# Kernel tuning notes

Hardware: AMD Instinct MI355X
Metric: run time of the kernel (lower is better)

Reference implementation:

```python
import jax, jax.numpy as jnp
import numpy as np

B, C, N, K = 2, 128, 4096, 16
DIM, PH, AH = 256, 64, 1024  # dim, pos_hidden_dim, dim*attn_hidden_multiplier
EPS = 1e-5

def _p(k, shape, scale=0.02):
    return jax.random.normal(k, shape, dtype=jnp.float32) * scale

def setup_inputs() -> dict:
    key0 = jax.random.key(0)
    ks = jax.random.split(key0, 32)
    d = {
        'pos': jax.random.normal(ks[0], (B, 3, N), dtype=jnp.float32),
        'key': jax.random.normal(ks[1], (B, C, N), dtype=jnp.float32),
        'query': jax.random.normal(ks[2], (B, C, N), dtype=jnp.float32),
        # MLP_Res on concat(key,query): in=2C, hidden=C, out=C
        'mlpv_w1': _p(ks[3], (C, 2 * C)), 'mlpv_b1': jnp.zeros((C,)),
        'mlpv_w2': _p(ks[4], (C, C)),     'mlpv_b2': jnp.zeros((C,)),
        'mlpv_ws': _p(ks[5], (C, 2 * C)), 'mlpv_bs': jnp.zeros((C,)),
        'wk': _p(ks[6], (DIM, C)), 'bk': jnp.zeros((DIM,)),
        'wq': _p(ks[7], (DIM, C)), 'bq': jnp.zeros((DIM,)),
        'wv': _p(ks[8], (DIM, C)), 'bv': jnp.zeros((DIM,)),
        # pos_mlp: Conv2d(3,PH,1) -> BN -> ReLU -> Conv2d(PH,DIM,1)
        'pos_w1': _p(ks[9], (PH, 3)),   'pos_b1': jnp.zeros((PH,)),
        'pos_g1': jnp.ones((PH,)),      'pos_be1': jnp.zeros((PH,)),
        'pos_w2': _p(ks[10], (DIM, PH)),'pos_b2': jnp.zeros((DIM,)),
        # attn_mlp: Conv2d(DIM,AH,1) -> BN -> ReLU -> Conv2d(AH,DIM,1)
        'att_w1': _p(ks[11], (AH, DIM)), 'att_b1': jnp.zeros((AH,)),
        'att_g1': jnp.ones((AH,)),       'att_be1': jnp.zeros((AH,)),
        'att_w2': _p(ks[12], (DIM, AH)), 'att_b2': jnp.zeros((DIM,)),
        'we': _p(ks[13], (C, DIM)), 'be': jnp.zeros((C,)),
    }
    return d

def conv1d(w, b, x):  # 1x1 conv: (o,i),(B,i,N)->(B,o,N)
    return jnp.einsum('oi,bin->bon', w, x) + b[None, :, None]

def conv2d(w, b, x):  # 1x1 conv: (o,i),(B,i,N,K)->(B,o,N,K)
    return jnp.einsum('oi,bink->bonk', w, x) + b[None, :, None, None]

def bn2d(g, be, x):  # training-mode batchnorm over (B,N,K) per channel
    m = x.mean(axis=(0, 2, 3), keepdims=True)
    v = x.var(axis=(0, 2, 3), keepdims=True)
    return g[None, :, None, None] * (x - m) * jax.lax.rsqrt(v + EPS) + be[None, :, None, None]

def knn_idx(pos, k):  # pos: (B,3,N) -> idx (B,N,k) of k nearest (incl. self)
    sq = jnp.sum(pos * pos, axis=1)                      # (B,N)
    d2 = sq[:, :, None] + sq[:, None, :] - 2.0 * jnp.einsum('bdn,bdm->bnm', pos, pos)
    _, idx = jax.lax.top_k(-d2, k)                       # smallest distances
    return idx

def group(x, idx):  # x:(B,C,N), idx:(B,N,K) -> (B,C,N,K)
    return jax.vmap(lambda xb, ib: xb[:, ib])(x, idx)

def reference(pos, key, query,
              mlpv_w1, mlpv_b1, mlpv_w2, mlpv_b2, mlpv_ws, mlpv_bs,
              wk, bk, wq, bq, wv, bv,
              pos_w1, pos_b1, pos_g1, pos_be1, pos_w2, pos_b2,
              att_w1, att_b1, att_g1, att_be1, att_w2, att_b2,
              we, be):
    x = jnp.concatenate([key, query], axis=1)            # (B,2C,N)
    value = conv1d(mlpv_w2, mlpv_b2, jax.nn.relu(conv1d(mlpv_w1, mlpv_b1, x))) \
            + conv1d(mlpv_ws, mlpv_bs, x)                # MLP_Res -> (B,C,N)
    identity = value
    k_f = conv1d(wk, bk, key)                            # (B,DIM,N)
    q_f = conv1d(wq, bq, query)
    v_f = conv1d(wv, bv, value)
    idx = knn_idx(pos, K)                                # (B,N,K)
    key_g = group(k_f, idx)                              # (B,DIM,N,K)
    qk_rel = q_f[:, :, :, None] - key_g
    pos_rel = pos[:, :, :, None] - group(pos, idx)       # (B,3,N,K)
    pos_emb = conv2d(pos_w2, pos_b2,
                     jax.nn.relu(bn2d(pos_g1, pos_be1, conv2d(pos_w1, pos_b1, pos_rel))))
    attn = conv2d(att_w2, att_b2,
                  jax.nn.relu(bn2d(att_g1, att_be1, conv2d(att_w1, att_b1, qk_rel + pos_emb))))
    attn = jax.nn.softmax(attn, axis=-1)                 # softmax over K neighbors
    v = v_f[:, :, :, None] + pos_emb                     # (B,DIM,N,K)
    agg = jnp.einsum('bcik,bcik->bci', attn, v)          # (B,DIM,N)
    y = conv1d(we, be, agg)
    return y + identity
```

## Files before the change

kernel.cpp:

```cpp
#include <hip/hip_runtime.h>
#include <math.h>

#define BB 2
#define CC 128
#define NN 4096
#define KK 16
#define DIMD 256
#define PHH 64
#define AHH 1024
#define EPSF 1e-5f
#define RSPLIT 128
#define RKCH ((BB * NN * KK) / RSPLIT)
#define LSTR 258
#define KNN_CAP 512
#define FPT 8

typedef unsigned short ushort_t;
typedef unsigned char uchar_t;
typedef unsigned long long u64;
typedef long long i64;
typedef __attribute__((ext_vector_type(8))) short short8;
typedef __attribute__((ext_vector_type(8))) unsigned short u16x8;
typedef __attribute__((ext_vector_type(4))) unsigned short u16x4;
typedef __attribute__((ext_vector_type(2))) unsigned short u16x2;
typedef __attribute__((ext_vector_type(4))) float f32x4;

__device__ __forceinline__ ushort_t f2b(float x) {
    union { float f; unsigned u; } v; v.f = x;
    unsigned r = v.u + 0x7fff + ((v.u >> 16) & 1);
    return (ushort_t)(r >> 16);
}
__device__ __forceinline__ float b2f(ushort_t x) {
    union { unsigned u; float f; } v; v.u = ((unsigned)x) << 16;
    return v.f;
}
__device__ __forceinline__ unsigned fsort(float x) {
    union { float f; unsigned u; } v; v.f = x;
    return v.u ^ ((v.u >> 31) ? 0xFFFFFFFFu : 0x80000000u);
}
__device__ __forceinline__ uchar_t f2f8(float x) {
    int p = __builtin_amdgcn_cvt_pk_fp8_f32(x, x, 0, false);
    return (uchar_t)(p & 0xFF);
}

#define GLDS16(gp, lp) __builtin_amdgcn_global_load_lds( \
    (const __attribute__((address_space(1))) void*)(gp), \
    (__attribute__((address_space(3))) void*)(lp), 16, 0, 0)

__global__ void zero_kernel(float* p, int n) {
    int i = blockIdx.x * blockDim.x + threadIdx.x;
    if (i < n) p[i] = 0.f;
}

__global__ __launch_bounds__(256) void knn_kernel(const float* __restrict__ pos,
                                                  int* __restrict__ idx) {
    int bid = blockIdx.x;
    int b = bid / NN, n = bid % NN;
    int t = threadIdx.x;
    int lane = t & 63, w = t >> 6;
    const float* px = pos + (size_t)b * 3 * NN;
    const float* py = px + NN;
    const float* pz = px + 2 * NN;
    float qx = px[n], qy = py[n], qz = pz[n];
    float qs = qx * qx + qy * qy + qz * qz;

    u64 keys[KK];
    u64 lmin = ~0ull;
#pragma unroll
    for (int j = 0; j < KK; ++j) {
        int m = t + 256 * j;
        float mx = px[m], my = py[m], mz = pz[m];
        float ms = mx * mx + my * my + mz * mz;
        float dt = qx * mx + qy * my + qz * mz;
        float d = qs + ms - 2.f * dt;
        u64 k = ((u64)fsort(d) << 32) | (unsigned)m;
        keys[j] = k;
        lmin = k < lmin ? k : lmin;
    }

    __shared__ u64 T0s[4];
    __shared__ u64 pool[KNN_CAP];
    __shared__ int cnt;

    u64 k = lmin, m4 = 0;
#pragma unroll
    for (int r = 0; r < 4; ++r) {
        u64 mv = k;
#pragma unroll
        for (int off = 32; off >= 1; off >>= 1) {
            u64 o = __shfl_xor(mv, off);
            mv = o < mv ? o : mv;
        }
        if (r == 3) m4 = mv;
        if (k == mv) k = ~0ull;
    }
    if (lane == 0) T0s[w] = m4;
    if (t == 0) cnt = 0;
    __syncthreads();
    u64 T0 = T0s[0];
    T0 = T0s[1] > T0 ? T0s[1] : T0;
    T0 = T0s[2] > T0 ? T0s[2] : T0;
    T0 = T0s[3] > T0 ? T0s[3] : T0;

#pragma unroll
    for (int j = 0; j < KK; ++j) {
        if (keys[j] <= T0) {
            int p = atomicAdd(&cnt, 1);
            if (p < KNN_CAP) pool[p] = keys[j];
        }
    }
    __syncthreads();
    int C = cnt < KNN_CAP ? cnt : KNN_CAP;
    if (t < C) {
        u64 me = pool[t];
        int r = 0;
        for (int i = 0; i < C; ++i) r += (pool[i] < me);
        if (r < KK) idx[(size_t)bid * KK + r] = (int)(me & 0xFFFFFFFFu);
    }
}

__global__ __launch_bounds__(256) void cvtx_kernel(const float* __restrict__ key,
                                                   const float* __restrict__ query,
                                                   ushort_t* __restrict__ kqT) {
    __shared__ float xs[128][65];
    int b = blockIdx.y, n0 = blockIdx.x * 64, t = threadIdx.x;
    for (int h = 0; h < 2; ++h) {
        const float* src = (h ? query : key) + (size_t)b * CC * NN;
        if (h) __syncthreads();
#pragma unroll
        for (int it = 0; it < 32; ++it) {
            int l = it * 256 + t;
            xs[l >> 6][l & 63] = src[(size_t)(l >> 6) * NN + n0 + (l & 63)];
        }
        __syncthreads();
#pragma unroll
        for (int it = 0; it < 8; ++it) {
            int l = it * 256 + t;
            int row = l >> 5, c0 = (l & 31) * 4;
            u16x4 pk;
            pk[0] = f2b(xs[c0][row]);
            pk[1] = f2b(xs[c0 + 1][row]);
            pk[2] = f2b(xs[c0 + 2][row]);
            pk[3] = f2b(xs[c0 + 3][row]);
            *(u16x4*)(kqT + ((size_t)b * NN + n0 + row) * 256 + h * 128 + c0) = pk;
        }
    }
}

template <int KLOOP, int ASTR, int EPI, int OSTR>
__global__ __launch_bounds__(256) void gemmT_kernel(const ushort_t* __restrict__ A,
                                                    const ushort_t* __restrict__ Bm,
                                                    const float* __restrict__ bias,
                                                    float* __restrict__ outF,
                                                    ushort_t* __restrict__ outB) {
    __shared__ ushort_t lA[128 * 32];
    __shared__ ushort_t lB[128 * 32];
    int t = threadIdx.x, lane = t & 63, w = t >> 6;
    int wr = w >> 1, wc = w & 1;
    size_t row0 = (size_t)blockIdx.x * 128;
    int col0 = blockIdx.y * 128;
    int m16 = lane & 15, kg = lane >> 4;
    f32x4 acc[4][4];
#pragma unroll
    for (int i = 0; i < 4; ++i)
#pragma unroll
        for (int j = 0; j < 4; ++j) acc[i][j] = (f32x4){0.f, 0.f, 0.f, 0.f};

    const ushort_t* gA = A + (row0 + (size_t)w * 16 + m16) * ASTR + kg * 8;
    const ushort_t* gB = Bm + ((size_t)(col0 + w * 16 + m16)) * KLOOP + kg * 8;
    ushort_t* lA0 = lA + w * 512;
    ushort_t* lB0 = lB + w * 512;
    for (int kt = 0; kt < KLOOP / 32; ++kt) {
        int ko = kt * 32;
        GLDS16(gA + ko, lA0);
        GLDS16(gA + (size_t)64 * ASTR + ko, lA0 + 2048);
        GLDS16(gB + ko, lB0);
        GLDS16(gB + (size_t)64 * KLOOP + ko, lB0 + 2048);
        __syncthreads();
        short8 af[4], bf[4];
#pragma unroll
        for (int i = 0; i < 4; ++i) {
            af[i] = *(const short8*)(lA + ((wr * 4 + i) * 512 + kg * 128 + m16 * 8));
            bf[i] = *(const short8*)(lB + ((wc * 4 + i) * 512 + kg * 128 + m16 * 8));
        }
#pragma unroll
        for (int i = 0; i < 4; ++i)
#pragma unroll
            for (int j = 0; j < 4; ++j)
                acc[i][j] = __builtin_amdgcn_mfma_f32_16x16x32_bf16(af[i], bf[j], acc[i][j], 0, 0, 0);
        __syncthreads();
    }
#pragma unroll
    for (int j = 0; j < 4; ++j) {
        int n = col0 + wc * 64 + j * 16 + m16;
        float bi = bias[n];
#pragma unroll
        for (int i = 0; i < 4; ++i) {
            size_t r = row0 + wr * 64 + i * 16 + kg * 4;
#pragma unroll
            for (int rg = 0; rg < 4; ++rg) {
                float v = acc[i][j][rg] + bi;
                if (EPI == 0) outB[(r + rg) * (size_t)OSTR + n] = f2b(fmaxf(v, 0.f));
                else          outF[(r + rg) * (size_t)OSTR + n] = v;
            }
        }
    }
}

__global__ __launch_bounds__(256) void gemmval_kernel(const ushort_t* __restrict__ kqT,
                                                      const ushort_t* __restrict__ h1T,
                                                      const ushort_t* __restrict__ wsb,
                                                      const ushort_t* __restrict__ w2vb,
                                                      const float* __restrict__ b2,
                                                      const float* __restrict__ bs,
                                                      float* __restrict__ valueTf,
                                                      ushort_t* __restrict__ valueTb) {
    __shared__ ushort_t lA[128 * 32];
    __shared__ ushort_t lB[128 * 32];
    int t = threadIdx.x, lane = t & 63, w = t >> 6;
    int wr = w >> 1, wc = w & 1;
    size_t row0 = (size_t)blockIdx.x * 128;
    int m16 = lane & 15, kg = lane >> 4;
    f32x4 acc[4][4];
#pragma unroll
    for (int i = 0; i < 4; ++i)
#pragma unroll
        for (int j = 0; j < 4; ++j) acc[i][j] = (f32x4){0.f, 0.f, 0.f, 0.f};
    ushort_t* lA0 = lA + w * 512;
    ushort_t* lB0 = lB + w * 512;

    {
        const ushort_t* gA = kqT + (row0 + (size_t)w * 16 + m16) * 256 + kg * 8;
        const ushort_t* gB = wsb + ((size_t)(w * 16 + m16)) * 256 + kg * 8;
        for (int kt = 0; kt < 8; ++kt) {
            int ko = kt * 32;
            GLDS16(gA + ko, lA0);
            GLDS16(gA + (size_t)64 * 256 + ko, lA0 + 2048);
            GLDS16(gB + ko, lB0);
            GLDS16(gB + (size_t)64 * 256 + ko, lB0 + 2048);
            __syncthreads();
            short8 af[4], bf[4];
#pragma unroll
            for (int i = 0; i < 4; ++i) {
                af[i] = *(const short8*)(lA + ((wr * 4 + i) * 512 + kg * 128 + m16 * 8));
                bf[i] = *(const short8*)(lB + ((wc * 4 + i) * 512 + kg * 128 + m16 * 8));
            }
#pragma unroll
            for (int i = 0; i < 4; ++i)
#pragma unroll
                for (int j = 0; j < 4; ++j)
                    acc[i][j] = __builtin_amdgcn_mfma_f32_16x16x32_bf16(af[i], bf[j], acc[i][j], 0, 0, 0);
            __syncthreads();
        }
    }
    {
        const ushort_t* gA = h1T + (row0 + (size_t)w * 16 + m16) * 128 + kg * 8;
        const ushort_t* gB = w2vb + ((size_t)(w * 16 + m16)) * 128 + kg * 8;
        for (int kt = 0; kt < 4; ++kt) {
            int ko = kt * 32;
            GLDS16(gA + ko, lA0);
            GLDS16(gA + (size_t)64 * 128 + ko, lA0 + 2048);
            GLDS16(gB + ko, lB0);
            GLDS16(gB + (size_t)64 * 128 + ko, lB0 + 2048);
            __syncthreads();
            short8 af[4], bf[4];
#pragma unroll
            for (int i = 0; i < 4; ++i) {
                af[i] = *(const short8*)(lA + ((wr * 4 + i) * 512 + kg * 128 + m16 * 8));
                bf[i] = *(const short8*)(lB + ((wc * 4 + i) * 512 + kg * 128 + m16 * 8));
            }
#pragma unroll
            for (int i = 0; i < 4; ++i)
#pragma unroll
                for (int j = 0; j < 4; ++j)
                    acc[i][j] = __builtin_amdgcn_mfma_f32_16x16x32_bf16(af[i], bf[j], acc[i][j], 0, 0, 0);
            __syncthreads();
        }
    }
#pragma unroll
    for (int j = 0; j < 4; ++j) {
        int n = wc * 64 + j * 16 + m16;
        float bi = b2[n] + bs[n];
#pragma unroll
        for (int i = 0; i < 4; ++i) {
            size_t r = row0 + wr * 64 + i * 16 + kg * 4;
#pragma unroll
            for (int rg = 0; rg < 4; ++rg) {
                float v = acc[i][j][rg] + bi;
                valueTf[(r + rg) * (size_t)CC + n] = v;
                valueTb[(r + rg) * (size_t)CC + n] = f2b(v);
            }
        }
    }
}

__global__ __launch_bounds__(256) void gemmkq_kernel(const ushort_t* __restrict__ kqT,
                                                     const ushort_t* __restrict__ wkb,
                                                     const ushort_t* __restrict__ wqb,
                                                     const float* __restrict__ bk,
                                                     const float* __restrict__ bq,
                                                     float* __restrict__ kT,
                                                     float* __restrict__ qT) {
    __shared__ ushort_t lA[128 * 32];
    __shared__ ushort_t lB[128 * 32];
    int half = blockIdx.y >> 1;
    int col0 = (blockIdx.y & 1) * 128;
    const ushort_t* A = kqT + half * 128;
    const ushort_t* Bm = half ? wqb : wkb;
    const float* bias = half ? bq : bk;
    float* outF = half ? qT : kT;

    int t = threadIdx.x, lane = t & 63, w = t >> 6;
    int wr = w >> 1, wc = w & 1;
    size_t row0 = (size_t)blockIdx.x * 128;
    int m16 = lane & 15, kg = lane >> 4;
    f32x4 acc[4][4];
#pragma unroll
    for (int i = 0; i < 4; ++i)
#pragma unroll
        for (int j = 0; j < 4; ++j) acc[i][j] = (f32x4){0.f, 0.f, 0.f, 0.f};
    const ushort_t* gA = A + (row0 + (size_t)w * 16 + m16) * 256 + kg * 8;
    const ushort_t* gB = Bm + ((size_t)(col0 + w * 16 + m16)) * 128 + kg * 8;
    ushort_t* lA0 = lA + w * 512;
    ushort_t* lB0 = lB + w * 512;
    for (int kt = 0; kt < 4; ++kt) {
        int ko = kt * 32;
        GLDS16(gA + ko, lA0);
        GLDS16(gA + (size_t)64 * 256 + ko, lA0 + 2048);
        GLDS16(gB + ko, lB0);
        GLDS16(gB + (size_t)64 * 128 + ko, lB0 + 2048);
        __syncthreads();
        short8 af[4], bf[4];
#pragma unroll
        for (int i = 0; i < 4; ++i) {
            af[i] = *(const short8*)(lA + ((wr * 4 + i) * 512 + kg * 128 + m16 * 8));
            bf[i] = *(const short8*)(lB + ((wc * 4 + i) * 512 + kg * 128 + m16 * 8));
        }
#pragma unroll
        for (int i = 0; i < 4; ++i)
#pragma unroll
            for (int j = 0; j < 4; ++j)
                acc[i][j] = __builtin_amdgcn_mfma_f32_16x16x32_bf16(af[i], bf[j], acc[i][j], 0, 0, 0);
        __syncthreads();
    }
#pragma unroll
    for (int j = 0; j < 4; ++j) {
        int n = col0 + wc * 64 + j * 16 + m16;
        float bi = bias[n];
#pragma unroll
        for (int i = 0; i < 4; ++i) {
            size_t r = row0 + wr * 64 + i * 16 + kg * 4;
#pragma unroll
            for (int rg = 0; rg < 4; ++rg)
                outF[(r + rg) * (size_t)DIMD + n] = acc[i][j][rg] + bi;
        }
    }
}

__global__ __launch_bounds__(256) void pos_stats_kernel(const float* __restrict__ pos,
                                                        const int* __restrict__ idx,
                                                        float* __restrict__ stats) {
    int sid = blockIdx.x * 256 + threadIdx.x;
    int b = sid / (NN * KK);
    int r = sid % (NN * KK);
    int n = r / KK;
    int m = idx[sid];
    const float* px = pos + (size_t)b * 3 * NN;
    float dx = px[n] - px[m];
    float dy = px[NN + n] - px[NN + m];
    float dz = px[2 * NN + n] - px[2 * NN + m];
    float v[9] = {dx, dy, dz, dx * dx, dy * dy, dz * dz, dx * dy, dx * dz, dy * dz};
    __shared__ float red[256];
    for (int j = 0; j < 9; ++j) {
        red[threadIdx.x] = v[j];
        __syncthreads();
        for (int off = 128; off >= 1; off >>= 1) {
            if (threadIdx.x < off) red[threadIdx.x] += red[threadIdx.x + off];
            __syncthreads();
        }
        if (threadIdx.x == 0) atomicAdd(&stats[j], red[0]);
        __syncthreads();
    }
}

__global__ void pos_bn_kernel(const float* __restrict__ stats, const float* __restrict__ pw1,
                              const float* __restrict__ pb1, const float* __restrict__ pg1,
                              const float* __restrict__ pbe1, float* __restrict__ posA) {
    int c = threadIdx.x;
    if (c >= PHH) return;
    float M = (float)(BB * NN * KK);
    float mu0 = stats[0] / M, mu1 = stats[1] / M, mu2 = stats[2] / M;
    float E00 = stats[3] / M, E11 = stats[4] / M, E22 = stats[5] / M;
    float E01 = stats[6] / M, E02 = stats[7] / M, E12 = stats[8] / M;
    float w0 = pw1[c * 3], w1 = pw1[c * 3 + 1], w2 = pw1[c * 3 + 2];
    float wmu = w0 * mu0 + w1 * mu1 + w2 * mu2;
    float mean_h = wmu + pb1[c];
    float Eh2 = w0 * w0 * E00 + w1 * w1 * E11 + w2 * w2 * E22
              + 2.f * (w0 * w1 * E01 + w0 * w2 * E02 + w1 * w2 * E12)
              + 2.f * pb1[c] * wmu + pb1[c] * pb1[c];
    float var = Eh2 - mean_h * mean_h;
    float a1 = pg1[c] * rsqrtf(var + EPSF);
    posA[c] = a1;
    posA[PHH + c] = pbe1[c] - mean_h * a1;
}

__global__ __launch_bounds__(256) void p1_kernel(const float* __restrict__ pos,
                                                 const int* __restrict__ idx,
                                                 const float* __restrict__ pw1,
                                                 const float* __restrict__ pb1,
                                                 const float* __restrict__ posA,
                                                 ushort_t* __restrict__ p1) {
    int gid = blockIdx.x * 256 + threadIdx.x;
    int samp = gid >> 6, c = gid & 63;
    int p = samp >> 4;
    int b = p >> 12, n = p & (NN - 1);
    int m = idx[samp];
    const float* px = pos + (size_t)b * 3 * NN;
    float dx = px[n] - px[m];
    float dy = px[NN + n] - px[NN + m];
    float dz = px[2 * NN + n] - px[2 * NN + m];
    float h = pw1[c * 3] * dx + pw1[c * 3 + 1] * dy + pw1[c * 3 + 2] * dz + pb1[c];
    p1[gid] = f2b(fmaxf(h * posA[c] + posA[PHH + c], 0.f));
}

__global__ __launch_bounds__(256) void mu_kernel(const ushort_t* __restrict__ sb16,
                                                 float* __restrict__ mu) {
    __shared__ float red[8][DIMD];
    int t = threadIdx.x;
    int rg = t >> 5;
    int c0 = (t & 31) * 8;
    const ushort_t* p = sb16 + ((size_t)blockIdx.x * 512 + rg * 64) * DIMD + c0;
    float a0 = 0.f, a1 = 0.f, a2 = 0.f, a3 = 0.f, a4 = 0.f, a5 = 0.f, a6 = 0.f, a7 = 0.f;
    for (int i = 0; i < 64; ++i) {
        u16x8 v = *(const u16x8*)(p + (size_t)i * DIMD);
        a0 += b2f(v[0]); a1 += b2f(v[1]); a2 += b2f(v[2]); a3 += b2f(v[3]);
        a4 += b2f(v[4]); a5 += b2f(v[5]); a6 += b2f(v[6]); a7 += b2f(v[7]);
    }
    red[rg][c0] = a0; red[rg][c0 + 1] = a1; red[rg][c0 + 2] = a2; red[rg][c0 + 3] = a3;
    red[rg][c0 + 4] = a4; red[rg][c0 + 5] = a5; red[rg][c0 + 6] = a6; red[rg][c0 + 7] = a7;
    __syncthreads();
    float s = 0.f;
#pragma unroll
    for (int g = 0; g < 8; ++g) s += red[g][t];
    atomicAdd(&mu[t], s);
}

__global__ __launch_bounds__(256) void rg_kernel(const ushort_t* __restrict__ S,
                                                 float* __restrict__ Rpart) {
    __shared__ ushort_t ls[32 * LSTR];
    int t = threadIdx.x;
    int lane = t & 63, w = t >> 6;
    int wr = w >> 1, wc = w & 1;
    int ti = blockIdx.y >> 1, tj = blockIdx.y & 1;
    int m16 = lane & 15, kg = lane >> 4;
    size_t kbase = (size_t)blockIdx.x * RKCH;

    f32x4 acc[4][4];
#pragma unroll
    for (int i = 0; i < 4; ++i)
#pragma unroll
        for (int j = 0; j < 4; ++j) acc[i][j] = (f32x4){0.f, 0.f, 0.f, 0.f};

    int lm = t >> 3;
    int lc = (t & 7) * 32;
    const ushort_t* gS = S + (kbase + lm) * DIMD + lc;
    ushort_t* lp = ls + lm * LSTR + lc;

    for (int kt = 0; kt < RKCH / 32; ++kt) {
        const ushort_t* gp = gS + (size_t)kt * 32 * DIMD;
        u16x8 v0 = *(const u16x8*)(gp);
        u16x8 v1 = *(const u16x8*)(gp + 8);
        u16x8 v2 = *(const u16x8*)(gp + 16);
        u16x8 v3 = *(const u16x8*)(gp + 24);
        __syncthreads();
#pragma unroll
        for (int q = 0; q < 4; ++q) {
            *(u16x2*)(lp + 0 + 2 * q) = (u16x2){v0[2 * q], v0[2 * q + 1]};
            *(u16x2*)(lp + 8 + 2 * q) = (u16x2){v1[2 * q], v1[2 * q + 1]};
            *(u16x2*)(lp + 16 + 2 * q) = (u16x2){v2[2 * q], v2[2 * q + 1]};
            *(u16x2*)(lp + 24 + 2 * q) = (u16x2){v3[2 * q], v3[2 * q + 1]};
        }
        __syncthreads();
        short8 af[4], bf[4];
#pragma unroll
        for (int i = 0; i < 4; ++i) {
            int chA = ti * 128 + wr * 64 + i * 16 + m16;
            int chB = tj * 128 + wc * 64 + i * 16 + m16;
#pragma unroll
            for (int j = 0; j < 8; ++j) {
                int k = kg * 8 + j;
                af[i][j] = (short)ls[k * LSTR + chA];
                bf[i][j] = (short)ls[k * LSTR + chB];
            }
        }
#pragma unroll
        for (int i = 0; i < 4; ++i)
#pragma unroll
            for (int j = 0; j < 4; ++j)
                acc[i][j] = __builtin_amdgcn_mfma_f32_16x16x32_bf16(af[i], bf[j], acc[i][j], 0, 0, 0);
    }

    float* rp = Rpart + (size_t)blockIdx.x * (DIMD * DIMD);
#pragma unroll
    for (int i = 0; i < 4; ++i) {
        int r0 = ti * 128 + wr * 64 + i * 16 + kg * 4;
#pragma unroll
        for (int j = 0; j < 4; ++j) {
            int cn = tj * 128 + wc * 64 + j * 16 + m16;
#pragma unroll
            for (int rg = 0; rg < 4; ++rg)
                rp[(size_t)(r0 + rg) * DIMD + cn] = acc[i][j][rg];
        }
    }
}

__global__ __launch_bounds__(256) void r_reduce_kernel(const float* __restrict__ Rpart,
                                                       float* __restrict__ R) {
    int e = blockIdx.x * 256 + threadIdx.x;
    float s = 0.f;
    for (int p = 0; p < RSPLIT; ++p) s += Rpart[(size_t)p * (DIMD * DIMD) + e];
    R[e] = s;
}

__global__ __launch_bounds__(256) void attn_bn_kernel(const float* __restrict__ R,
                                                      const float* __restrict__ mu,
                                                      const float* __restrict__ aw1,
                                                      const float* __restrict__ ab1,
                                                      const float* __restrict__ ag1,
                                                      const float* __restrict__ abe1,
                                                      float* __restrict__ attA) {
    int c = blockIdx.x;
    int t = threadIdx.x;
    __shared__ float wsh[DIMD];
    __shared__ float red[DIMD];
    wsh[t] = aw1[(size_t)c * DIMD + t];
    __syncthreads();
    const float* Rr = R + (size_t)t * DIMD;
    float q = 0.f;
#pragma unroll 4
    for (int j = 0; j < DIMD; ++j) q += Rr[j] * wsh[j];
    red[t] = q * wsh[t];
    __syncthreads();
    for (int off = 128; off >= 1; off >>= 1) {
        if (t < off) red[t] += red[t + off];
        __syncthreads();
    }
    float wRw = red[0];
    __syncthreads();
    red[t] = wsh[t] * mu[t];
    __syncthreads();
    for (int off = 128; off >= 1; off >>= 1) {
        if (t < off) red[t] += red[t + off];
        __syncthreads();
    }
    if (t == 0) {
        float M = (float)(BB * NN * KK);
        float wmu = red[0] / M;
        float b1c = ab1[c];
        float Eh = wmu + b1c;
        float Eh2 = wRw / M + 2.f * b1c * wmu + b1c * b1c;
        float var = Eh2 - Eh * Eh;
        float a1 = ag1[c] * rsqrtf(var + EPSF);
        attA[c] = a1;
        attA[AHH + c] = a1 * b1c + abe1[c] - Eh * a1;
    }
}

__global__ void cvt_w_kernel(const float* __restrict__ aw1, const float* __restrict__ aw2,
                             const float* __restrict__ pw2,
                             const float* __restrict__ mw1, const float* __restrict__ mws,
                             const float* __restrict__ mw2,
                             const float* __restrict__ wk, const float* __restrict__ wq,
                             const float* __restrict__ wv,
                             ushort_t* __restrict__ w1b, ushort_t* __restrict__ w2b,
                             ushort_t* __restrict__ pw2b,
                             ushort_t* __restrict__ w1vb, ushort_t* __restrict__ wsvb,
                             ushort_t* __restrict__ w2vb,
                             ushort_t* __restrict__ wkb, ushort_t* __restrict__ wqb,
                             ushort_t* __restrict__ wvb,
                             uchar_t* __restrict__ w2f8) {
    int i = blockIdx.x * 256 + threadIdx.x;
    int o = i;
    if (o < 262144) { w1b[o] = f2b(aw1[o]); return; }   o -= 262144;
    if (o < 262144) { w2b[o] = f2b(aw2[o]); w2f8[o] = f2f8(aw2[o] * 64.f); return; } o -= 262144;
    if (o < 16384)  { pw2b[o] = f2b(pw2[o]); return; }  o -= 16384;
    if (o < 32768)  { w1vb[o] = f2b(mw1[o]); return; }  o -= 32768;
    if (o < 32768)  { wsvb[o] = f2b(mws[o]); return; }  o -= 32768;
    if (o < 16384)  { w2vb[o] = f2b(mw2[o]); return; }  o -= 16384;
    if (o < 32768)  { wkb[o] = f2b(wk[o]); return; }    o -= 32768;
    if (o < 32768)  { wqb[o] = f2b(wq[o]); return; }    o -= 32768;
    if (o < 32768)  { wvb[o] = f2b(wv[o]); }
}

template <int KDIM>
__global__ __launch_bounds__(256) void gemmS_kernel(const ushort_t* __restrict__ A,
                                                    const ushort_t* __restrict__ Bm,
                                                    const float* __restrict__ p0,
                                                    ushort_t* __restrict__ Sb,
                                                    const float* __restrict__ qT,
                                                    const float* __restrict__ kT,
                                                    const int* __restrict__ gidx) {
    __shared__ ushort_t lA[128 * 32];
    __shared__ ushort_t lB[128 * 32];
    int t = threadIdx.x;
    int lane = t & 63, w = t >> 6;
    int wr = w >> 1, wc = w & 1;
    size_t row0 = (size_t)blockIdx.x * 128;
    int col0 = blockIdx.y * 128;
    int m16 = lane & 15, kg = lane >> 4;

    f32x4 acc[4][4];
#pragma unroll
    for (int i = 0; i < 4; ++i)
#pragma unroll
        for (int j = 0; j < 4; ++j) acc[i][j] = (f32x4){0.f, 0.f, 0.f, 0.f};

    const ushort_t* gA = A + (row0 + (size_t)w * 16 + m16) * KDIM + kg * 8;
    const ushort_t* gB = Bm + ((size_t)(col0 + w * 16 + m16)) * KDIM + kg * 8;
    ushort_t* lA0 = lA + w * 512;
    ushort_t* lB0 = lB + w * 512;

    for (int kt = 0; kt < KDIM / 32; ++kt) {
        int ko = kt * 32;
        GLDS16(gA + ko, lA0);
        GLDS16(gA + (size_t)64 * KDIM + ko, lA0 + 2048);
        GLDS16(gB + ko, lB0);
        GLDS16(gB + (size_t)64 * KDIM + ko, lB0 + 2048);
        __syncthreads();
        short8 af[4], bf[4];
#pragma unroll
        for (int i = 0; i < 4; ++i) {
            af[i] = *(const short8*)(lA + ((wr * 4 + i) * 512 + kg * 128 + m16 * 8));
            bf[i] = *(const short8*)(lB + ((wc * 4 + i) * 512 + kg * 128 + m16 * 8));
        }
#pragma unroll
        for (int i = 0; i < 4; ++i)
#pragma unroll
            for (int j = 0; j < 4; ++j)
                acc[i][j] = __builtin_amdgcn_mfma_f32_16x16x32_bf16(af[i], bf[j], acc[i][j], 0, 0, 0);
        __syncthreads();
    }

    int nn[4]; float bi[4];
#pragma unroll
    for (int j = 0; j < 4; ++j) { nn[j] = col0 + wc * 64 + j * 16 + m16; bi[j] = p0[nn[j]]; }
#pragma unroll
    for (int i = 0; i < 4; ++i) {
        size_t r = row0 + wr * 64 + i * 16 + kg * 4;
#pragma unroll
        for (int rg = 0; rg < 4; ++rg) {
            size_t rr = r + rg;
            int p = (int)(rr >> 4);
            int krow = (p & ~(NN - 1)) + gidx[rr];
            const float* qrow = qT + (size_t)p * DIMD;
            const float* kro = kT + (size_t)krow * DIMD;
#pragma unroll
            for (int j = 0; j < 4; ++j) {
                float sv = qrow[nn[j]] - kro[nn[j]] + acc[i][j][rg] + bi[j];
                Sb[rr * (size_t)DIMD + nn[j]] = f2b(sv);
            }
        }
    }
}

__global__ __launch_bounds__(256, 3) void fused_mlp_kernel(const ushort_t* __restrict__ S,
                                                        const ushort_t* __restrict__ w1b,
                                                        const uchar_t* __restrict__ w2f8,
                                                        const float* __restrict__ attA,
                                                        const float* __restrict__ ab2,
                                                        const int* __restrict__ idx,
                                                        const float* __restrict__ qT,
                                                        const float* __restrict__ kT,
                                                        const float* __restrict__ vT,
                                                        float* __restrict__ aggT) {
    __shared__ char smem[40960];
    ushort_t* lS  = (ushort_t*)smem;
    uchar_t*  lHt = (uchar_t*)(smem + 32768);
    ushort_t* lgB = (ushort_t*)smem;

    int t = threadIdx.x;
    int lane = t & 63, w = t >> 6;
    int m16 = lane & 15, kg = lane >> 4;
    size_t row0 = (size_t)blockIdx.x * 64;

#pragma unroll
    for (int i = 0; i < 8; ++i) {
        int lb = w * 8 + i;
        int kt = lb >> 2, st = lb & 3;
        const ushort_t* gp = S + (row0 + st * 16 + m16) * DIMD + kt * 32 + kg * 8;
        GLDS16(gp, lS + lb * 512);
    }

    f32x4 acc2[4][4];
#pragma unroll
    for (int i = 0; i < 4; ++i)
#pragma unroll
        for (int j = 0; j < 4; ++j) acc2[i][j] = (f32x4){0.f, 0.f, 0.f, 0.f};

    __syncthreads();

    for (int jc = 0; jc < 8; ++jc) {
        f32x4 acc1[2][4];
#pragma unroll
        for (int hi = 0; hi < 2; ++hi)
#pragma unroll
            for (int sj = 0; sj < 4; ++sj) acc1[hi][sj] = (f32x4){0.f, 0.f, 0.f, 0.f};
#pragma unroll
        for (int kt = 0; kt < 8; ++kt) {
            short8 af[2], bf[4];
#pragma unroll
            for (int hi = 0; hi < 2; ++hi)
                af[hi] = *(const short8*)(w1b + ((size_t)(jc * 128 + w * 32 + hi * 16 + m16)) * DIMD + kt * 32 + kg * 8);
#pragma unroll
            for (int sj = 0; sj < 4; ++sj)
                bf[sj] = *(const short8*)(lS + (kt * 4 + sj) * 512 + kg * 128 + m16 * 8);
#pragma unroll
            for (int hi = 0; hi < 2; ++hi)
#pragma unroll
                for (int sj = 0; sj < 4; ++sj)
                    acc1[hi][sj] = __builtin_amdgcn_mfma_f32_16x16x32_bf16(af[hi], bf[sj], acc1[hi][sj], 0, 0, 0);
        }
        __syncthreads();
#pragma unroll
        for (int hi = 0; hi < 2; ++hi) {
            float4 sc4 = *(const float4*)(attA + jc * 128 + w * 32 + hi * 16 + kg * 4);
            float4 of4 = *(const float4*)(attA + AHH + jc * 128 + w * 32 + hi * 16 + kg * 4);
#pragma unroll
            for (int sj = 0; sj < 4; ++sj) {
                float h0 = fmaxf(sc4.x * acc1[hi][sj][0] + of4.x, 0.f);
                float h1 = fmaxf(sc4.y * acc1[hi][sj][1] + of4.y, 0.f);
                float h2 = fmaxf(sc4.z * acc1[hi][sj][2] + of4.z, 0.f);
                float h3 = fmaxf(sc4.w * acc1[hi][sj][3] + of4.w, 0.f);
                int p01 = __builtin_amdgcn_cvt_pk_fp8_f32(h0, h1, 0, false);
                int pk = __builtin_amdgcn_cvt_pk_fp8_f32(h2, h3, p01, true);
                int ah = (w * 4 + sj) * 512 + (hi * 2 + (kg >> 1)) * 128 + m16 * 8 + (kg & 1) * 4;
                *(int*)(lHt + ah) = pk;
            }
        }
        __syncthreads();
#pragma unroll
        for (int g = 0; g < 4; ++g) {
            i64 af2[4], bf2[4];
#pragma unroll
            for (int oi = 0; oi < 4; ++oi)
                af2[oi] = *(const i64*)(w2f8 + ((size_t)(w * 64 + oi * 16 + m16)) * AHH + jc * 128 + g * 32 + kg * 8);
#pragma unroll
            for (int sj = 0; sj < 4; ++sj)
                bf2[sj] = *(const i64*)(lHt + (g * 4 + sj) * 512 + kg * 128 + m16 * 8);
#pragma unroll
            for (int oi = 0; oi < 4; ++oi)
#pragma unroll
                for (int sj = 0; sj < 4; ++sj)
                    acc2[oi][sj] = __builtin_amdgcn_mfma_f32_16x16x32_fp8_fp8(af2[oi], bf2[sj], acc2[oi][sj], 0, 0, 0);
        }
    }
    __syncthreads();

    const float invsc = 0.015625f;
#pragma unroll
    for (int oi = 0; oi < 4; ++oi) {
        int ob = w * 64 + oi * 16 + kg * 4;
        float4 b2v = *(const float4*)(ab2 + ob);
#pragma unroll
        for (int sj = 0; sj < 4; ++sj) {
            int smp = sj * 16 + m16;
            lgB[(ob + 0) * 72 + smp] = f2b(acc2[oi][sj][0] * invsc + b2v.x);
            lgB[(ob + 1) * 72 + smp] = f2b(acc2[oi][sj][1] * invsc + b2v.y);
            lgB[(ob + 2) * 72 + smp] = f2b(acc2[oi][sj][2] * invsc + b2v.z);
            lgB[(ob + 3) * 72 + smp] = f2b(acc2[oi][sj][3] * invsc + b2v.w);
        }
    }
    __syncthreads();

    int out = t;
    for (int pt = 0; pt < 4; ++pt) {
        int pid = (int)(row0 >> 4) + pt;
        u16x8 v0 = *(const u16x8*)(lgB + out * 72 + pt * 16);
        u16x8 v1 = *(const u16x8*)(lgB + out * 72 + pt * 16 + 8);
        float lg[KK];
#pragma unroll
        for (int s = 0; s < 8; ++s) { lg[s] = b2f(v0[s]); lg[s + 8] = b2f(v1[s]); }
        float mx = lg[0];
#pragma unroll
        for (int s = 1; s < KK; ++s) mx = fmaxf(mx, lg[s]);
        float se = 0.f;
#pragma unroll
        for (int s = 0; s < KK; ++s) { lg[s] = expf(lg[s] - mx); se += lg[s]; }
        float inv = 1.f / se;
        int base = pid & ~(NN - 1);
        float acc = 0.f;
#pragma unroll
        for (int s = 0; s < KK; ++s) {
            int row = pid * KK + s;
            int krow = base + idx[row];
            float sv = b2f(S[(size_t)row * DIMD + out]);
            float kv = kT[(size_t)krow * DIMD + out];
            acc += lg[s] * (sv + kv);
        }
        float vf = vT[(size_t)pid * DIMD + out];
        float q  = qT[(size_t)pid * DIMD + out];
        aggT[(size_t)pid * DIMD + out] = vf - q + acc * inv;
    }
}

__global__ __launch_bounds__(256) void final_kernel(const float* __restrict__ aggT,
                                                    const float* __restrict__ we,
                                                    const float* __restrict__ be,
                                                    const float* __restrict__ valueTf,
                                                    float* __restrict__ out) {
    __shared__ float xs[2 * FPT][DIMD];
    __shared__ float vs[2 * FPT][CC];
    int b = blockIdx.y;
    int n0 = blockIdx.x * (2 * FPT);
    int t = threadIdx.x;
    const float4* src = (const float4*)(aggT + ((size_t)b * NN + n0) * DIMD);
    float4* dst = (float4*)xs;
#pragma unroll
    for (int l = 0; l < (2 * FPT * DIMD / 4) / 256; ++l) dst[t + 256 * l] = src[t + 256 * l];
    const float4* src2 = (const float4*)(valueTf + ((size_t)b * NN + n0) * CC);
    float4* dst2 = (float4*)vs;
#pragma unroll
    for (int l = 0; l < (2 * FPT * CC / 4) / 256; ++l) dst2[t + 256 * l] = src2[t + 256 * l];
    __syncthreads();
    int o = t & 127, ph = t >> 7;
    float acc[FPT];
#pragma unroll
    for (int p = 0; p < FPT; ++p) acc[p] = 0.f;
    const float4* wr = (const float4*)(we + (size_t)o * DIMD);
#pragma unroll 8
    for (int i4 = 0; i4 < DIMD / 4; ++i4) {
        float4 w4 = wr[i4];
#pragma unroll
        for (int p = 0; p < FPT; ++p) {
            float4 x4 = *(const float4*)&xs[ph * FPT + p][i4 * 4];
            acc[p] += w4.x * x4.x + w4.y * x4.y + w4.z * x4.z + w4.w * x4.w;
        }
    }
    float bo = be[o];
#pragma unroll
    for (int p = 0; p < FPT; ++p) {
        size_t oi = ((size_t)b * CC + o) * NN + n0 + ph * FPT + p;
        out[oi] = acc[p] + bo + vs[ph * FPT + p][o];
    }
}

extern "C" void kernel_launch(void* const* d_in, const int* in_sizes, int n_in,
                              void* d_out, int out_size, void* d_ws, size_t ws_size,
                              hipStream_t stream) {
    (void)in_sizes; (void)n_in; (void)out_size; (void)ws_size;
    const float* pos     = (const float*)d_in[0];
    const float* key     = (const float*)d_in[1];
    const float* query   = (const float*)d_in[2];
    const float* mlpv_w1 = (const float*)d_in[3];
    const float* mlpv_b1 = (const float*)d_in[4];
    const float* mlpv_w2 = (const float*)d_in[5];
    const float* mlpv_b2 = (const float*)d_in[6];
    const float* mlpv_ws = (const float*)d_in[7];
    const float* mlpv_bs = (const float*)d_in[8];
    const float* wk  = (const float*)d_in[9];
    const float* bk  = (const float*)d_in[10];
    const float* wq  = (const float*)d_in[11];
    const float* bq  = (const float*)d_in[12];
    const float* wv  = (const float*)d_in[13];
    const float* bv  = (const float*)d_in[14];
    const float* pw1 = (const float*)d_in[15];
    const float* pb1 = (const float*)d_in[16];
    const float* pg1 = (const float*)d_in[17];
    const float* pbe1= (const float*)d_in[18];
    const float* pw2 = (const float*)d_in[19];
    const float* pb2 = (const float*)d_in[20];
    const float* aw1 = (const float*)d_in[21];
    const float* ab1 = (const float*)d_in[22];
    const float* ag1 = (const float*)d_in[23];
    const float* abe1= (const float*)d_in[24];
    const float* aw2 = (const float*)d_in[25];
    const float* ab2 = (const float*)d_in[26];
    const float* we  = (const float*)d_in[27];
    const float* be  = (const float*)d_in[28];
    float* out = (float*)d_out;

    char* wsb = (char*)d_ws;
    size_t off = 0;
    auto alloc = [&](size_t bytes) {
        void* p = wsb + off;
        off += (bytes + 255) & ~(size_t)255;
        return p;
    };
    const size_t M = (size_t)BB * NN * KK;
    const size_t P = (size_t)BB * NN;
    int*   idx   = (int*)  alloc(M * 4);
    ushort_t* kqT     = (ushort_t*)alloc(P * 256 * 2);
    ushort_t* h1T     = (ushort_t*)alloc(P * CC * 2);
    float*    valueTf = (float*)   alloc(P * CC * 4);
    ushort_t* valueTb = (ushort_t*)alloc(P * CC * 2);
    float* kT    = (float*)alloc(P * DIMD * 4);
    float* qT    = (float*)alloc(P * DIMD * 4);
    float* vT    = (float*)alloc(P * DIMD * 4);
    float* aggT  = (float*)alloc(P * DIMD * 4);
    float* zero0 = (float*)alloc((size_t)(16 + 256 + 65536) * 4);
    float* stats = zero0;
    float* mu    = zero0 + 16;
    float* R     = zero0 + 16 + 256;
    float* posA  = (float*)alloc((size_t)2 * PHH * 4);
    float* attA  = (float*)alloc((size_t)2 * AHH * 4);
    ushort_t* w1b  = (ushort_t*)alloc((size_t)AHH * DIMD * 2);
    ushort_t* w2b  = (ushort_t*)alloc((size_t)DIMD * AHH * 2);
    uchar_t*  w2f8 = (uchar_t*) alloc((size_t)DIMD * AHH);
    ushort_t* pw2b = (ushort_t*)alloc((size_t)DIMD * PHH * 2);
    ushort_t* w1vb = (ushort_t*)alloc((size_t)CC * 256 * 2);
    ushort_t* wsvb = (ushort_t*)alloc((size_t)CC * 256 * 2);
    ushort_t* w2vb = (ushort_t*)alloc((size_t)CC * CC * 2);
    ushort_t* wkb  = (ushort_t*)alloc((size_t)DIMD * CC * 2);
    ushort_t* wqb  = (ushort_t*)alloc((size_t)DIMD * CC * 2);
    ushort_t* wvb  = (ushort_t*)alloc((size_t)DIMD * CC * 2);
    ushort_t* sb16 = (ushort_t*)alloc(M * DIMD * 2);
    char* ovl = (char*)alloc((size_t)RSPLIT * DIMD * DIMD * 4);
    ushort_t* p1buf = (ushort_t*)ovl;
    float*    Rpart = (float*)ovl;

    int ZN = 16 + 256 + 65536;
    zero_kernel<<<(ZN + 255) / 256, 256, 0, stream>>>(zero0, ZN);
    knn_kernel<<<BB * NN, 256, 0, stream>>>(pos, idx);
    cvt_w_kernel<<<(720896 + 255) / 256, 256, 0, stream>>>(aw1, aw2, pw2, mlpv_w1, mlpv_ws, mlpv_w2,
                                                           wk, wq, wv, w1b, w2b, pw2b,
                                                           w1vb, wsvb, w2vb, wkb, wqb, wvb, w2f8);
    cvtx_kernel<<<dim3(NN / 64, BB), 256, 0, stream>>>(key, query, kqT);
    gemmT_kernel<256, 256, 0, 128><<<dim3(P / 128, 1), 256, 0, stream>>>(kqT, w1vb, mlpv_b1, nullptr, h1T);
    gemmval_kernel<<<dim3(P / 128, 1), 256, 0, stream>>>(kqT, h1T, wsvb, w2vb, mlpv_b2, mlpv_bs, valueTf, valueTb);
    gemmkq_kernel<<<dim3(P / 128, 4), 256, 0, stream>>>(kqT, wkb, wqb, bk, bq, kT, qT);
    gemmT_kernel<128, 128, 1, 256><<<dim3(P / 128, 2), 256, 0, stream>>>(valueTb, wvb, bv, vT, nullptr);
    pos_stats_kernel<<<BB * NN * KK / 256, 256, 0, stream>>>(pos, idx, stats);
    pos_bn_kernel<<<1, 64, 0, stream>>>(stats, pw1, pb1, pg1, pbe1, posA);
    p1_kernel<<<(int)(M * PHH / 256), 256, 0, stream>>>(pos, idx, pw1, pb1, posA, p1buf);
    gemmS_kernel<PHH><<<dim3(M / 128, DIMD / 128), 256, 0, stream>>>(p1buf, pw2b, pb2, sb16, qT, kT, idx);
    mu_kernel<<<(int)(M / 512), 256, 0, stream>>>(sb16, mu);
    rg_kernel<<<dim3(RSPLIT, 4), 256, 0, stream>>>(sb16, Rpart);
    r_reduce_kernel<<<DIMD * DIMD / 256, 256, 0, stream>>>(Rpart, R);
    attn_bn_kernel<<<AHH, DIMD, 0, stream>>>(R, mu, aw1, ab1, ag1, abe1, attA);
    fused_mlp_kernel<<<(int)(M / 64), 256, 0, stream>>>(sb16, w1b, w2f8, attA, ab2, idx, qT, kT, vT, aggT);
    final_kernel<<<dim3(NN / (2 * FPT), BB), 256, 0, stream>>>(aggT, we, be, valueTf, out);
}
```

Before: 684.4 us.

## Run attention first-layer GEMM in FP8 with FP8 copy of S

The first attention-MLP GEMM in the fused kernel now uses FP8 MFMA instead of bf16. The weights are pre-scaled by 64 into FP8 and the scale is folded back into the BN coefficient. gemmS now writes an extra FP8 copy of S, which the fused kernel stages into padded shared memory with plain loads. This halves operand bytes and shared-memory footprint, at the cost of an extra global write in gemmS and reduced numerical precision. RSPLIT is also halved, shrinking the partial-reduction buffer and the number of partial sums to reduce.

```diff
diff --git a/kernel.cpp b/kernel.cpp
--- a/kernel.cpp
+++ b/kernel.cpp
@@ -9,7 +9,7 @@
 #define PHH 64
 #define AHH 1024
 #define EPSF 1e-5f
-#define RSPLIT 128
+#define RSPLIT 64
 #define RKCH ((BB * NN * KK) / RSPLIT)
 #define LSTR 258
 #define KNN_CAP 512
@@ -23,6 +23,8 @@
 typedef __attribute__((ext_vector_type(8))) unsigned short u16x8;
 typedef __attribute__((ext_vector_type(4))) unsigned short u16x4;
 typedef __attribute__((ext_vector_type(2))) unsigned short u16x2;
+typedef __attribute__((ext_vector_type(2))) unsigned int u32x2;
+typedef __attribute__((ext_vector_type(4))) unsigned int u32x4;
 typedef __attribute__((ext_vector_type(4))) float f32x4;
 
 __device__ __forceinline__ ushort_t f2b(float x) {
@@ -561,7 +563,7 @@
         float Eh2 = wRw / M + 2.f * b1c * wmu + b1c * b1c;
         float var = Eh2 - Eh * Eh;
         float a1 = ag1[c] * rsqrtf(var + EPSF);
-        attA[c] = a1;
+        attA[c] = a1 * 0.015625f;
         attA[AHH + c] = a1 * b1c + abe1[c] - Eh * a1;
     }
 }
@@ -572,7 +574,7 @@
                              const float* __restrict__ mw2,
                              const float* __restrict__ wk, const float* __restrict__ wq,
                              const float* __restrict__ wv,
-                             ushort_t* __restrict__ w1b, ushort_t* __restrict__ w2b,
+                             uchar_t* __restrict__ w1f8, ushort_t* __restrict__ w2b,
                              ushort_t* __restrict__ pw2b,
                              ushort_t* __restrict__ w1vb, ushort_t* __restrict__ wsvb,
                              ushort_t* __restrict__ w2vb,
@@ -581,7 +583,7 @@
                              uchar_t* __restrict__ w2f8) {
     int i = blockIdx.x * 256 + threadIdx.x;
     int o = i;
-    if (o < 262144) { w1b[o] = f2b(aw1[o]); return; }   o -= 262144;
+    if (o < 262144) { w1f8[o] = f2f8(aw1[o] * 64.f); return; }   o -= 262144;
     if (o < 262144) { w2b[o] = f2b(aw2[o]); w2f8[o] = f2f8(aw2[o] * 64.f); return; } o -= 262144;
     if (o < 16384)  { pw2b[o] = f2b(pw2[o]); return; }  o -= 16384;
     if (o < 32768)  { w1vb[o] = f2b(mw1[o]); return; }  o -= 32768;
@@ -597,6 +599,7 @@
                                                     const ushort_t* __restrict__ Bm,
                                                     const float* __restrict__ p0,
                                                     ushort_t* __restrict__ Sb,
+                                                    uchar_t* __restrict__ Sf8,
                                                     const float* __restrict__ qT,
                                                     const float* __restrict__ kT,
                                                     const int* __restrict__ gidx) {
@@ -658,13 +661,15 @@
             for (int j = 0; j < 4; ++j) {
                 float sv = qrow[nn[j]] - kro[nn[j]] + acc[i][j][rg] + bi[j];
                 Sb[rr * (size_t)DIMD + nn[j]] = f2b(sv);
+                Sf8[rr * (size_t)DIMD + nn[j]] = f2f8(sv);
             }
         }
     }
 }
 
 __global__ __launch_bounds__(256, 3) void fused_mlp_kernel(const ushort_t* __restrict__ S,
-                                                        const ushort_t* __restrict__ w1b,
+                                                        const uchar_t* __restrict__ Sf8,
+                                                        const uchar_t* __restrict__ w1f8,
                                                         const uchar_t* __restrict__ w2f8,
                                                         const float* __restrict__ attA,
                                                         const float* __restrict__ ab2,
@@ -673,9 +678,9 @@
                                                         const float* __restrict__ kT,
                                                         const float* __restrict__ vT,
                                                         float* __restrict__ aggT) {
-    __shared__ char smem[40960];
-    ushort_t* lS  = (ushort_t*)smem;
-    uchar_t*  lHt = (uchar_t*)(smem + 32768);
+    __shared__ char smem[36992];
+    uchar_t*  lS  = (uchar_t*)smem;
+    uchar_t*  lHt = (uchar_t*)(smem + 20480);
     ushort_t* lgB = (ushort_t*)smem;
 
     int t = threadIdx.x;
@@ -683,12 +688,19 @@
     int m16 = lane & 15, kg = lane >> 4;
     size_t row0 = (size_t)blockIdx.x * 64;
 
-#pragma unroll
-    for (int i = 0; i < 8; ++i) {
-        int lb = w * 8 + i;
-        int kt = lb >> 2, st = lb & 3;
-        const ushort_t* gp = S + (row0 + st * 16 + m16) * DIMD + kt * 32 + kg * 8;
-        GLDS16(gp, lS + lb * 512);
+    {
+        int smp = t >> 2, q = t & 3;
+        int sj = smp >> 4, m16s = smp & 15;
+        const uchar_t* gp = Sf8 + (row0 + smp) * DIMD + q * 64;
+#pragma unroll
+        for (int i = 0; i < 4; ++i) {
+            int k0 = q * 64 + i * 16;
+            int kt = k0 >> 5, kk = k0 & 31;
+            u32x4 v = *(const u32x4*)(gp + i * 16);
+            int base = (kt * 4 + sj) * 640 + m16s * 40 + kk;
+            *(u32x2*)(lS + base) = (u32x2){v[0], v[1]};
+            *(u32x2*)(lS + base + 8) = (u32x2){v[2], v[3]};
+        }
     }
 
     f32x4 acc2[4][4];
@@ -707,18 +719,18 @@
             for (int sj = 0; sj < 4; ++sj) acc1[hi][sj] = (f32x4){0.f, 0.f, 0.f, 0.f};
 #pragma unroll
         for (int kt = 0; kt < 8; ++kt) {
-            short8 af[2], bf[4];
+            i64 af[2], bf[4];
 #pragma unroll
             for (int hi = 0; hi < 2; ++hi)
-                af[hi] = *(const short8*)(w1b + ((size_t)(jc * 128 + w * 32 + hi * 16 + m16)) * DIMD + kt * 32 + kg * 8);
+                af[hi] = *(const i64*)(w1f8 + ((size_t)(jc * 128 + w * 32 + hi * 16 + m16)) * DIMD + kt * 32 + kg * 8);
 #pragma unroll
             for (int sj = 0; sj < 4; ++sj)
-                bf[sj] = *(const short8*)(lS + (kt * 4 + sj) * 512 + kg * 128 + m16 * 8);
+                bf[sj] = *(const i64*)(lS + (kt * 4 + sj) * 640 + m16 * 40 + kg * 8);
 #pragma unroll
             for (int hi = 0; hi < 2; ++hi)
 #pragma unroll
                 for (int sj = 0; sj < 4; ++sj)
-                    acc1[hi][sj] = __builtin_amdgcn_mfma_f32_16x16x32_bf16(af[hi], bf[sj], acc1[hi][sj], 0, 0, 0);
+                    acc1[hi][sj] = __builtin_amdgcn_mfma_f32_16x16x32_fp8_fp8(af[hi], bf[sj], acc1[hi][sj], 0, 0, 0);
         }
         __syncthreads();
 #pragma unroll
@@ -903,7 +915,7 @@
     float* R     = zero0 + 16 + 256;
     float* posA  = (float*)alloc((size_t)2 * PHH * 4);
     float* attA  = (float*)alloc((size_t)2 * AHH * 4);
-    ushort_t* w1b  = (ushort_t*)alloc((size_t)AHH * DIMD * 2);
+    uchar_t*  w1f8 = (uchar_t*) alloc((size_t)AHH * DIMD);
     ushort_t* w2b  = (ushort_t*)alloc((size_t)DIMD * AHH * 2);
     uchar_t*  w2f8 = (uchar_t*) alloc((size_t)DIMD * AHH);
     ushort_t* pw2b = (ushort_t*)alloc((size_t)DIMD * PHH * 2);
@@ -914,6 +926,7 @@
     ushort_t* wqb  = (ushort_t*)alloc((size_t)DIMD * CC * 2);
     ushort_t* wvb  = (ushort_t*)alloc((size_t)DIMD * CC * 2);
     ushort_t* sb16 = (ushort_t*)alloc(M * DIMD * 2);
+    uchar_t*  Sf8  = (uchar_t*) alloc(M * DIMD);
     char* ovl = (char*)alloc((size_t)RSPLIT * DIMD * DIMD * 4);
     ushort_t* p1buf = (ushort_t*)ovl;
     float*    Rpart = (float*)ovl;
@@ -922,7 +935,7 @@
     zero_kernel<<<(ZN + 255) / 256, 256, 0, stream>>>(zero0, ZN);
     knn_kernel<<<BB * NN, 256, 0, stream>>>(pos, idx);
     cvt_w_kernel<<<(720896 + 255) / 256, 256, 0, stream>>>(aw1, aw2, pw2, mlpv_w1, mlpv_ws, mlpv_w2,
-                                                           wk, wq, wv, w1b, w2b, pw2b,
+                                                           wk, wq, wv, w1f8, w2b, pw2b,
                                                            w1vb, wsvb, w2vb, wkb, wqb, wvb, w2f8);
     cvtx_kernel<<<dim3(NN / 64, BB), 256, 0, stream>>>(key, query, kqT);
     gemmT_kernel<256, 256, 0, 128><<<dim3(P / 128, 1), 256, 0, stream>>>(kqT, w1vb, mlpv_b1, nullptr, h1T);
@@ -932,11 +945,11 @@
     pos_stats_kernel<<<BB * NN * KK / 256, 256, 0, stream>>>(pos, idx, stats);
     pos_bn_kernel<<<1, 64, 0, stream>>>(stats, pw1, pb1, pg1, pbe1, posA);
     p1_kernel<<<(int)(M * PHH / 256), 256, 0, stream>>>(pos, idx, pw1, pb1, posA, p1buf);
-    gemmS_kernel<PHH><<<dim3(M / 128, DIMD / 128), 256, 0, stream>>>(p1buf, pw2b, pb2, sb16, qT, kT, idx);
+    gemmS_kernel<PHH><<<dim3(M / 128, DIMD / 128), 256, 0, stream>>>(p1buf, pw2b, pb2, sb16, Sf8, qT, kT, idx);
     mu_kernel<<<(int)(M / 512), 256, 0, stream>>>(sb16, mu);
     rg_kernel<<<dim3(RSPLIT, 4), 256, 0, stream>>>(sb16, Rpart);
     r_reduce_kernel<<<DIMD * DIMD / 256, 256, 0, stream>>>(Rpart, R);
     attn_bn_kernel<<<AHH, DIMD, 0, stream>>>(R, mu, aw1, ab1, ag1, abe1, attA);
-    fused_mlp_kernel<<<(int)(M / 64), 256, 0, stream>>>(sb16, w1b, w2f8, attA, ab2, idx, qT, kT, vT, aggT);
+    fused_mlp_kernel<<<(int)(M / 64), 256, 0, stream>>>(sb16, Sf8, w1f8, w2f8, attA, ab2, idx, qT, kT, vT, aggT);
     final_kernel<<<dim3(NN / (2 * FPT), BB), 256, 0, stream>>>(aggT, we, be, valueTf, out);
 }
```

New measurement: 715.0 us. 4.5% more time.
